# Optimization experiments

Measured on AMD Instinct MI355X. Metric: run time of the kernel, lower is better.

The kernel has to match this reference:

```python
import jax, jax.numpy as jnp
import numpy as np

N_NODES = 50000
N_EDGES = 800000
F_IN, F_LAT, F_OUT = 64, 64, 64


def _graph_conv(x, W, b, src, dst, deg_out_isqrt, deg_in_isqrt):
    # DGL GraphConv, norm='both': D_out^{-1/2} scaling on src side,
    # linear transform (mult-first since in_feats >= out_feats),
    # scatter-sum to dst, D_in^{-1/2} scaling on dst side, + bias.
    n = x.shape[0]
    h = (x * deg_out_isqrt[:, None]) @ W              # [N, F_out]
    msg = h[src]                                      # [E, F_out] gather
    agg = jax.ops.segment_sum(msg, dst, num_segments=n)  # [N, F_out] scatter
    return agg * deg_in_isqrt[:, None] + b


def setup_inputs() -> dict:
    key = jax.random.key(0)
    ks = jax.random.split(key, 6)
    x = jax.random.normal(ks[0], (N_NODES, F_IN), dtype=jnp.float32)
    W1 = jax.random.normal(ks[1], (F_IN, F_LAT), dtype=jnp.float32) / np.sqrt(F_IN)
    b1 = jnp.zeros((F_LAT,), dtype=jnp.float32)
    W2 = jax.random.normal(ks[2], (F_LAT, F_OUT), dtype=jnp.float32) / np.sqrt(F_LAT)
    b2 = jnp.zeros((F_OUT,), dtype=jnp.float32)
    src = jax.random.randint(ks[3], (N_EDGES,), 0, N_NODES, dtype=jnp.int32)
    dst = jax.random.randint(ks[4], (N_EDGES,), 0, N_NODES, dtype=jnp.int32)
    return {"x": x, "W1": W1, "b1": b1, "W2": W2, "b2": b2, "src": src, "dst": dst}


def reference(x, W1, b1, W2, b2, src, dst):
    n = x.shape[0]
    ones = jnp.ones((src.shape[0],), dtype=x.dtype)
    deg_out = jax.ops.segment_sum(ones, src, num_segments=n)
    deg_in = jax.ops.segment_sum(ones, dst, num_segments=n)
    deg_out_isqrt = jnp.where(deg_out > 0, jax.lax.rsqrt(jnp.maximum(deg_out, 1.0)), 0.0)
    deg_in_isqrt = jnp.where(deg_in > 0, jax.lax.rsqrt(jnp.maximum(deg_in, 1.0)), 0.0)
    h = _graph_conv(x, W1, b1, src, dst, deg_out_isqrt, deg_in_isqrt)
    h = jax.nn.relu(h)
    out = _graph_conv(h, W2, b2, src, dst, deg_out_isqrt, deg_in_isqrt)
    return out
```

## Files before the change

kernel.cpp:

```cpp
#include <hip/hip_runtime.h>

#define NF 64
#define BC 64
#define RANGE 16384
#define RWORDS (RANGE / 4)

typedef __attribute__((ext_vector_type(8))) short short8;
typedef __attribute__((ext_vector_type(4))) float floatx4;

__device__ __forceinline__ unsigned short f2bf(float f) {
  unsigned int u = __float_as_uint(f);
  return (unsigned short)((u + 0x7fffu + ((u >> 16) & 1u)) >> 16);
}

__global__ __launch_bounds__(256) void hist_kernel(
    const int* __restrict__ src, const int* __restrict__ dst,
    unsigned char* __restrict__ Gout, unsigned char* __restrict__ Gin,
    unsigned char* __restrict__ rank, int n, int nE, int R, int chunk) {
  __shared__ int cnt[RWORDS];
  const int rb = blockIdx.x % (R * BC);
  const int kind = blockIdx.x / (R * BC);
  const int r = rb / BC, b = rb % BC;
  const int r0 = r * RANGE;
  for (int i = threadIdx.x; i < RWORDS; i += 256) cnt[i] = 0;
  __syncthreads();
  const int lo = b * chunk, hi = min(lo + chunk, nE);
  const int* keys = kind ? src : dst;
  const int n4 = (hi > lo) ? ((hi - lo) >> 2) : 0;
  const int4* keys4 = (const int4*)(keys + lo);
  if (kind == 0) {
    for (int i = threadIdx.x; i < n4; i += 256) {
      int4 v = keys4[i];
      int e0 = lo + 4 * i;
      unsigned int k, old, sh;
      k = (unsigned int)(v.x - r0);
      if (k < (unsigned int)RANGE) { sh = (k & 3) * 8; old = atomicAdd(&cnt[k >> 2], 1u << sh); rank[e0 + 0] = (unsigned char)(old >> sh); }
      k = (unsigned int)(v.y - r0);
      if (k < (unsigned int)RANGE) { sh = (k & 3) * 8; old = atomicAdd(&cnt[k >> 2], 1u << sh); rank[e0 + 1] = (unsigned char)(old >> sh); }
      k = (unsigned int)(v.z - r0);
      if (k < (unsigned int)RANGE) { sh = (k & 3) * 8; old = atomicAdd(&cnt[k >> 2], 1u << sh); rank[e0 + 2] = (unsigned char)(old >> sh); }
      k = (unsigned int)(v.w - r0);
      if (k < (unsigned int)RANGE) { sh = (k & 3) * 8; old = atomicAdd(&cnt[k >> 2], 1u << sh); rank[e0 + 3] = (unsigned char)(old >> sh); }
    }
    for (int e = lo + 4 * n4 + threadIdx.x; e < hi; e += 256) {
      unsigned int k = (unsigned int)(keys[e] - r0);
      if (k < (unsigned int)RANGE) {
        unsigned int sh = (k & 3) * 8;
        unsigned int old = atomicAdd(&cnt[k >> 2], 1u << sh);
        rank[e] = (unsigned char)(old >> sh);
      }
    }
    __syncthreads();
    unsigned int* Gw = (unsigned int*)(Gin + (size_t)b * n + r0);
    for (int i = threadIdx.x; i < RWORDS; i += 256)
      if (r0 + 4 * i < n) Gw[i] = (unsigned int)cnt[i];
  } else {
    for (int i = threadIdx.x; i < n4; i += 256) {
      int4 v = keys4[i];
      unsigned int k;
      k = (unsigned int)(v.x - r0);
      if (k < (unsigned int)RANGE) atomicAdd(&cnt[k >> 2], 1u << ((k & 3) * 8));
      k = (unsigned int)(v.y - r0);
      if (k < (unsigned int)RANGE) atomicAdd(&cnt[k >> 2], 1u << ((k & 3) * 8));
      k = (unsigned int)(v.z - r0);
      if (k < (unsigned int)RANGE) atomicAdd(&cnt[k >> 2], 1u << ((k & 3) * 8));
      k = (unsigned int)(v.w - r0);
      if (k < (unsigned int)RANGE) atomicAdd(&cnt[k >> 2], 1u << ((k & 3) * 8));
    }
    for (int e = lo + 4 * n4 + threadIdx.x; e < hi; e += 256) {
      unsigned int k = (unsigned int)(keys[e] - r0);
      if (k < (unsigned int)RANGE) atomicAdd(&cnt[k >> 2], 1u << ((k & 3) * 8));
    }
    __syncthreads();
    unsigned int* Gw = (unsigned int*)(Gout + (size_t)b * n + r0);
    for (int i = threadIdx.x; i < RWORDS; i += 256)
      if (r0 + 4 * i < n) Gw[i] = (unsigned int)cnt[i];
  }
}

__global__ __launch_bounds__(256) void colscan_scan1_kernel(
    unsigned char* __restrict__ Gin, const unsigned char* __restrict__ Gout,
    float* __restrict__ so, float* __restrict__ si,
    int* __restrict__ lscan, int* __restrict__ bsum, int n) {
  __shared__ int s[256];
  const int tid = threadIdx.x;
  const int i = blockIdx.x * 256 + tid;
  int di = 0;
  if (i < n) {
    int base = 0;
    #pragma unroll 8
    for (int b = 0; b < BC; ++b) {
      int c = Gin[(size_t)b * n + i];
      Gin[(size_t)b * n + i] = (unsigned char)base;
      base += c;
    }
    di = base;
    int dsum = 0;
    #pragma unroll 8
    for (int b = 0; b < BC; ++b) dsum += Gout[(size_t)b * n + i];
    si[i] = di > 0 ? rsqrtf((float)di) : 0.f;
    so[i] = dsum > 0 ? rsqrtf((float)dsum) : 0.f;
  }
  s[tid] = di;
  __syncthreads();
  #pragma unroll
  for (int off = 1; off < 256; off <<= 1) {
    int t2 = (tid >= off) ? s[tid - off] : 0;
    __syncthreads();
    s[tid] += t2;
    __syncthreads();
  }
  if (i < n) lscan[i] = s[tid] - di;
  if (tid == 255) bsum[blockIdx.x] = s[255];
}

__global__ __launch_bounds__(256) void scan3_kernel(
    const int* __restrict__ lscan, const int* __restrict__ bsum,
    int* __restrict__ row_start, int n, int nE) {
  __shared__ int red[256];
  const int tid = threadIdx.x;
  const int b = blockIdx.x;
  red[tid] = (tid < b) ? bsum[tid] : 0;
  __syncthreads();
  #pragma unroll
  for (int s = 128; s > 0; s >>= 1) {
    if (tid < s) red[tid] += red[tid + s];
    __syncthreads();
  }
  const int off = red[0];
  const int i = b * 256 + tid;
  if (b == 0 && tid == 0) row_start[n] = nE;
  if (i < n) row_start[i] = lscan[i] + off;
}

__global__ __launch_bounds__(256) void basefill_kernel(
    const int* __restrict__ row_start, const unsigned char* __restrict__ Gin,
    int* __restrict__ base, int n, int nb) {
  const int c = blockIdx.x / nb;
  const int i = (blockIdx.x % nb) * 256 + threadIdx.x;
  if (i < n) base[(size_t)c * n + i] = row_start[i] + (int)Gin[(size_t)c * n + i];
}

__device__ __forceinline__ void mfma_gemm_core(
    const unsigned short* __restrict__ Ab, const unsigned short* __restrict__ Wt,
    unsigned short* __restrict__ H, int row0, int n, int t) {
  const int w = t >> 6, lane = t & 63;
  const int quad = lane >> 4, l15 = lane & 15;
  const short8 a0 = *(const short8*)&Ab[(w * 16 + l15) * 72 + quad * 8];
  const short8 a1 = *(const short8*)&Ab[(w * 16 + l15) * 72 + 32 + quad * 8];
  #pragma unroll
  for (int cg = 0; cg < 4; ++cg) {
    const short8 b0 = *(const short8*)&Wt[(cg * 16 + l15) * 72 + quad * 8];
    const short8 b1 = *(const short8*)&Wt[(cg * 16 + l15) * 72 + 32 + quad * 8];
    floatx4 acc = {0.f, 0.f, 0.f, 0.f};
    acc = __builtin_amdgcn_mfma_f32_16x16x32_bf16(a0, b0, acc, 0, 0, 0);
    acc = __builtin_amdgcn_mfma_f32_16x16x32_bf16(a1, b1, acc, 0, 0, 0);
    #pragma unroll
    for (int reg = 0; reg < 4; ++reg) {
      int grow = row0 + w * 16 + quad * 4 + reg;
      if (grow < n) H[(size_t)grow * NF + cg * 16 + l15] = f2bf(acc[reg]);
    }
  }
}

__device__ __forceinline__ void stage_wt(
    const float* __restrict__ W, unsigned short* __restrict__ Wt, int t) {
  #pragma unroll
  for (int i = 0; i < 16; ++i) {
    int idx = t + 256 * i;
    int k = idx >> 6, j = idx & 63;
    Wt[j * 72 + k] = f2bf(W[idx]);
  }
}

__global__ __launch_bounds__(256) void place_gemm1_kernel(
    const float* __restrict__ A, const float* __restrict__ so,
    const float* __restrict__ W, unsigned short* __restrict__ H, int n, int ggrid,
    const int* __restrict__ src, const int* __restrict__ dst,
    const unsigned char* __restrict__ rank, const int* __restrict__ base,
    unsigned short* __restrict__ sorted, int nE, int chunk) {
  __shared__ __align__(16) unsigned short Ab[64 * 72];
  __shared__ __align__(16) unsigned short Wt[64 * 72];
  const int t = threadIdx.x;
  if ((int)blockIdx.x >= ggrid) {
    int e = (blockIdx.x - ggrid) * 256 + t;
    if (e < nE) {
      int d = dst[e];
      int b = e / chunk;
      sorted[base[(size_t)b * n + d] + (int)rank[e]] = (unsigned short)src[e];
    }
    return;
  }
  stage_wt(W, Wt, t);
  const int row0 = blockIdx.x * 64;
  #pragma unroll
  for (int i = 0; i < 4; ++i) {
    int idx = t + 256 * i;
    int r = idx >> 4, c4 = idx & 15;
    int gr = row0 + r;
    float4 v = {0.f, 0.f, 0.f, 0.f};
    float s = 0.f;
    if (gr < n) {
      v = *(const float4*)&A[(size_t)gr * NF + c4 * 4];
      s = so[gr];
    }
    ushort4 o;
    o.x = f2bf(v.x * s); o.y = f2bf(v.y * s);
    o.z = f2bf(v.z * s); o.w = f2bf(v.w * s);
    *(ushort4*)&Ab[r * 72 + c4 * 4] = o;
  }
  __syncthreads();
  mfma_gemm_core(Ab, Wt, H, row0, n, t);
}

__global__ __launch_bounds__(256) void gemm2_kernel(
    const unsigned short* __restrict__ Tb, const float* __restrict__ W,
    unsigned short* __restrict__ H, int n) {
  __shared__ __align__(16) unsigned short Ab[64 * 72];
  __shared__ __align__(16) unsigned short Wt[64 * 72];
  const int t = threadIdx.x;
  stage_wt(W, Wt, t);
  const int row0 = blockIdx.x * 64;
  #pragma unroll
  for (int i = 0; i < 4; ++i) {
    int idx = t + 256 * i;
    int r = idx >> 4, c4 = idx & 15;
    int gr = row0 + r;
    ushort4 v = {0, 0, 0, 0};
    if (gr < n) v = *(const ushort4*)&Tb[(size_t)gr * NF + c4 * 4];
    *(ushort4*)&Ab[r * 72 + c4 * 4] = v;
  }
  __syncthreads();
  mfma_gemm_core(Ab, Wt, H, row0, n, t);
}

__device__ __forceinline__ void gather_sum(
    const unsigned short* __restrict__ H, const unsigned short* __restrict__ srcs,
    int beg, int end, int g, int c, float* acc) {
  const float4* Hv = (const float4*)H;
  int e = beg;
  for (; e + 16 <= end; e += 16) {
    int ia = srcs[e + g];
    int ib = srcs[e + 8 + g];
    float4 va = Hv[(size_t)ia * 8 + c];
    float4 vb = Hv[(size_t)ib * 8 + c];
    const unsigned int* pa = (const unsigned int*)&va;
    const unsigned int* pb = (const unsigned int*)&vb;
    #pragma unroll
    for (int k = 0; k < 4; ++k) {
      acc[2 * k]     += __uint_as_float(pa[k] << 16) + __uint_as_float(pb[k] << 16);
      acc[2 * k + 1] += __uint_as_float(pa[k] & 0xffff0000u) + __uint_as_float(pb[k] & 0xffff0000u);
    }
  }
  if (e + 8 <= end) {
    int ia = srcs[e + g];
    float4 va = Hv[(size_t)ia * 8 + c];
    const unsigned int* pa = (const unsigned int*)&va;
    #pragma unroll
    for (int k = 0; k < 4; ++k) {
      acc[2 * k]     += __uint_as_float(pa[k] << 16);
      acc[2 * k + 1] += __uint_as_float(pa[k] & 0xffff0000u);
    }
    e += 8;
  }
  if (e < end) {
    int idx = (e + g < end) ? (e + g) : (end - 1);
    float m = (e + g < end) ? 1.f : 0.f;
    int ia = srcs[idx];
    float4 va = Hv[(size_t)ia * 8 + c];
    const unsigned int* pa = (const unsigned int*)&va;
    #pragma unroll
    for (int k = 0; k < 4; ++k) {
      acc[2 * k]     += m * __uint_as_float(pa[k] << 16);
      acc[2 * k + 1] += m * __uint_as_float(pa[k] & 0xffff0000u);
    }
  }
  #pragma unroll
  for (int d = 8; d <= 32; d <<= 1) {
    #pragma unroll
    for (int k = 0; k < 8; ++k) acc[k] += __shfl_xor(acc[k], d);
  }
}

__global__ __launch_bounds__(256) void agg1_kernel(
    const unsigned short* __restrict__ H1, const int* __restrict__ row_start,
    const unsigned short* __restrict__ srcs, const float* __restrict__ si,
    const float* __restrict__ so, const float* __restrict__ b1,
    unsigned short* __restrict__ T, int n) {
  int node = blockIdx.x * 4 + (threadIdx.x >> 6);
  if (node >= n) return;
  const int lane = threadIdx.x & 63;
  const int g = lane >> 3;
  const int c = lane & 7;
  float acc[8] = {0, 0, 0, 0, 0, 0, 0, 0};
  gather_sum(H1, srcs, row_start[node], row_start[node + 1], g, c, acc);
  if (g == 0) {
    const float sin = si[node];
    const float son = so[node];
    ushort4 o0, o1;
    float v;
    v = fmaxf(fmaf(acc[0], sin, b1[c * 8 + 0]), 0.f) * son; o0.x = f2bf(v);
    v = fmaxf(fmaf(acc[1], sin, b1[c * 8 + 1]), 0.f) * son; o0.y = f2bf(v);
    v = fmaxf(fmaf(acc[2], sin, b1[c * 8 + 2]), 0.f) * son; o0.z = f2bf(v);
    v = fmaxf(fmaf(acc[3], sin, b1[c * 8 + 3]), 0.f) * son; o0.w = f2bf(v);
    v = fmaxf(fmaf(acc[4], sin, b1[c * 8 + 4]), 0.f) * son; o1.x = f2bf(v);
    v = fmaxf(fmaf(acc[5], sin, b1[c * 8 + 5]), 0.f) * son; o1.y = f2bf(v);
    v = fmaxf(fmaf(acc[6], sin, b1[c * 8 + 6]), 0.f) * son; o1.z = f2bf(v);
    v = fmaxf(fmaf(acc[7], sin, b1[c * 8 + 7]), 0.f) * son; o1.w = f2bf(v);
    *(ushort4*)&T[(size_t)node * NF + c * 8]     = o0;
    *(ushort4*)&T[(size_t)node * NF + c * 8 + 4] = o1;
  }
}

__global__ __launch_bounds__(256) void agg2_kernel(
    const unsigned short* __restrict__ H2, const int* __restrict__ row_start,
    const unsigned short* __restrict__ srcs, const float* __restrict__ si,
    const float* __restrict__ b2, float* __restrict__ out, int n) {
  int node = blockIdx.x * 4 + (threadIdx.x >> 6);
  if (node >= n) return;
  const int lane = threadIdx.x & 63;
  const int g = lane >> 3;
  const int c = lane & 7;
  float acc[8] = {0, 0, 0, 0, 0, 0, 0, 0};
  gather_sum(H2, srcs, row_start[node], row_start[node + 1], g, c, acc);
  if (g == 0) {
    const float sin = si[node];
    const float4 b4a = *(const float4*)&b2[c * 8];
    const float4 b4b = *(const float4*)&b2[c * 8 + 4];
    float4 r0, r1;
    r0.x = fmaf(acc[0], sin, b4a.x);
    r0.y = fmaf(acc[1], sin, b4a.y);
    r0.z = fmaf(acc[2], sin, b4a.z);
    r0.w = fmaf(acc[3], sin, b4a.w);
    r1.x = fmaf(acc[4], sin, b4b.x);
    r1.y = fmaf(acc[5], sin, b4b.y);
    r1.z = fmaf(acc[6], sin, b4b.z);
    r1.w = fmaf(acc[7], sin, b4b.w);
    *(float4*)&out[(size_t)node * NF + c * 8]     = r0;
    *(float4*)&out[(size_t)node * NF + c * 8 + 4] = r1;
  }
}

extern "C" void kernel_launch(void* const* d_in, const int* in_sizes, int n_in,
                              void* d_out, int out_size, void* d_ws, size_t ws_size,
                              hipStream_t stream) {
  const float* x  = (const float*)d_in[0];
  const float* W1 = (const float*)d_in[1];
  const float* b1 = (const float*)d_in[2];
  const float* W2 = (const float*)d_in[3];
  const float* b2 = (const float*)d_in[4];
  const int* src  = (const int*)d_in[5];
  const int* dst  = (const int*)d_in[6];
  float* out = (float*)d_out;

  const int N = in_sizes[0] / NF;
  const int E = in_sizes[5];
  const int NB = (N + 255) / 256;
  const int R  = (N + RANGE - 1) / RANGE;
  const int CH = (((E + BC - 1) / BC) + 3) & ~3;
  (void)ws_size;

  char* ws = (char*)d_ws;
  size_t p = 0;
  auto alloc = [&](size_t bytes) -> void* {
    void* r = ws + p;
    p = (p + bytes + 255) & ~(size_t)255;
    return r;
  };
  float* so         = (float*)alloc((size_t)N * 4);
  float* si         = (float*)alloc((size_t)N * 4);
  int*   row_start  = (int*)  alloc((size_t)(N + 1) * 4);
  int*   bsum       = (int*)  alloc((size_t)NB * 4);
  int*   lscan      = (int*)  alloc((size_t)N * 4);
  unsigned short* sorted_u16 = (unsigned short*)alloc((size_t)E * 2);
  unsigned char*  rank  = (unsigned char*)alloc((size_t)E);
  unsigned short* h1    = (unsigned short*)alloc((size_t)N * NF * 2);
  unsigned char*  G_in  = (unsigned char*)alloc((size_t)BC * N);
  unsigned char*  G_out = (unsigned char*)alloc((size_t)BC * N);
  unsigned short* tb    = (unsigned short*)alloc((size_t)N * NF * 2);
  int*            base  = (int*)alloc((size_t)BC * N * 4);
  unsigned short* h2 = h1;

  hist_kernel<<<2 * R * BC, 256, 0, stream>>>(src, dst, G_out, G_in, rank,
                                              N, E, R, CH);

  colscan_scan1_kernel<<<NB, 256, 0, stream>>>(G_in, G_out, so, si,
                                               lscan, bsum, N);

  scan3_kernel<<<NB, 256, 0, stream>>>(lscan, bsum, row_start, N, E);

  basefill_kernel<<<BC * NB, 256, 0, stream>>>(row_start, G_in, base, N, NB);

  const int ggrid = (N + 63) / 64;
  const int pgrid = (E + 255) / 256;
  const int agrid = (N + 3) / 4;

  place_gemm1_kernel<<<ggrid + pgrid, 256, 0, stream>>>(
      x, so, W1, h1, N, ggrid, src, dst, rank, base, sorted_u16, E, CH);

  agg1_kernel<<<agrid, 256, 0, stream>>>(h1, row_start, sorted_u16, si, so, b1, tb, N);

  gemm2_kernel<<<ggrid, 256, 0, stream>>>(tb, W2, h2, N);

  agg2_kernel<<<agrid, 256, 0, stream>>>(h2, row_start, sorted_u16, si, b2, out, N);
}
```

Measured before the change: 183.8 us.

## Fuse second GEMM into aggregation, merge scan with basefill, halve histogram chunks

Layer 2 now aggregates the scaled activations first and applies W2 per node afterwards, using an FP32 shared-memory matvec inside agg2. This removes the separate gemm2 kernel and the h2 round trip. The scan3 and basefill kernels are merged into one launch. The histogram uses 32 chunks with 512-thread blocks, down from 64 chunks with 256 threads. The cost is a 64x64 matvec per node computed on scalar FP32 in the aggregation kernel, a 16 KB W2 load per block, and a block-wide sync.

```diff
diff --git a/kernel.cpp b/kernel.cpp
--- a/kernel.cpp
+++ b/kernel.cpp
@@ -1,7 +1,7 @@
 #include <hip/hip_runtime.h>
 
 #define NF 64
-#define BC 64
+#define BC 32
 #define RANGE 16384
 #define RWORDS (RANGE / 4)
 
@@ -13,7 +13,7 @@
   return (unsigned short)((u + 0x7fffu + ((u >> 16) & 1u)) >> 16);
 }
 
-__global__ __launch_bounds__(256) void hist_kernel(
+__global__ __launch_bounds__(512) void hist_kernel(
     const int* __restrict__ src, const int* __restrict__ dst,
     unsigned char* __restrict__ Gout, unsigned char* __restrict__ Gin,
     unsigned char* __restrict__ rank, int n, int nE, int R, int chunk) {
@@ -22,14 +22,14 @@
   const int kind = blockIdx.x / (R * BC);
   const int r = rb / BC, b = rb % BC;
   const int r0 = r * RANGE;
-  for (int i = threadIdx.x; i < RWORDS; i += 256) cnt[i] = 0;
+  for (int i = threadIdx.x; i < RWORDS; i += 512) cnt[i] = 0;
   __syncthreads();
   const int lo = b * chunk, hi = min(lo + chunk, nE);
   const int* keys = kind ? src : dst;
   const int n4 = (hi > lo) ? ((hi - lo) >> 2) : 0;
   const int4* keys4 = (const int4*)(keys + lo);
   if (kind == 0) {
-    for (int i = threadIdx.x; i < n4; i += 256) {
+    for (int i = threadIdx.x; i < n4; i += 512) {
       int4 v = keys4[i];
       int e0 = lo + 4 * i;
       unsigned int k, old, sh;
@@ -42,7 +42,7 @@
       k = (unsigned int)(v.w - r0);
       if (k < (unsigned int)RANGE) { sh = (k & 3) * 8; old = atomicAdd(&cnt[k >> 2], 1u << sh); rank[e0 + 3] = (unsigned char)(old >> sh); }
     }
-    for (int e = lo + 4 * n4 + threadIdx.x; e < hi; e += 256) {
+    for (int e = lo + 4 * n4 + threadIdx.x; e < hi; e += 512) {
       unsigned int k = (unsigned int)(keys[e] - r0);
       if (k < (unsigned int)RANGE) {
         unsigned int sh = (k & 3) * 8;
@@ -52,10 +52,10 @@
     }
     __syncthreads();
     unsigned int* Gw = (unsigned int*)(Gin + (size_t)b * n + r0);
-    for (int i = threadIdx.x; i < RWORDS; i += 256)
+    for (int i = threadIdx.x; i < RWORDS; i += 512)
       if (r0 + 4 * i < n) Gw[i] = (unsigned int)cnt[i];
   } else {
-    for (int i = threadIdx.x; i < n4; i += 256) {
+    for (int i = threadIdx.x; i < n4; i += 512) {
       int4 v = keys4[i];
       unsigned int k;
       k = (unsigned int)(v.x - r0);
@@ -67,13 +67,13 @@
       k = (unsigned int)(v.w - r0);
       if (k < (unsigned int)RANGE) atomicAdd(&cnt[k >> 2], 1u << ((k & 3) * 8));
     }
-    for (int e = lo + 4 * n4 + threadIdx.x; e < hi; e += 256) {
+    for (int e = lo + 4 * n4 + threadIdx.x; e < hi; e += 512) {
       unsigned int k = (unsigned int)(keys[e] - r0);
       if (k < (unsigned int)RANGE) atomicAdd(&cnt[k >> 2], 1u << ((k & 3) * 8));
     }
     __syncthreads();
     unsigned int* Gw = (unsigned int*)(Gout + (size_t)b * n + r0);
-    for (int i = threadIdx.x; i < RWORDS; i += 256)
+    for (int i = threadIdx.x; i < RWORDS; i += 512)
       if (r0 + 4 * i < n) Gw[i] = (unsigned int)cnt[i];
   }
 }
@@ -114,13 +114,15 @@
   if (tid == 255) bsum[blockIdx.x] = s[255];
 }
 
-__global__ __launch_bounds__(256) void scan3_kernel(
+__global__ __launch_bounds__(256) void scan3_basefill_kernel(
     const int* __restrict__ lscan, const int* __restrict__ bsum,
-    int* __restrict__ row_start, int n, int nE) {
+    const unsigned char* __restrict__ Gin, int* __restrict__ row_start,
+    int* __restrict__ base, int n, int nb, int nE) {
   __shared__ int red[256];
   const int tid = threadIdx.x;
-  const int b = blockIdx.x;
-  red[tid] = (tid < b) ? bsum[tid] : 0;
+  const int c = blockIdx.x / nb;
+  const int ib = blockIdx.x % nb;
+  red[tid] = (tid < ib) ? bsum[tid] : 0;
   __syncthreads();
   #pragma unroll
   for (int s = 128; s > 0; s >>= 1) {
@@ -128,17 +130,13 @@
     __syncthreads();
   }
   const int off = red[0];
-  const int i = b * 256 + tid;
-  if (b == 0 && tid == 0) row_start[n] = nE;
-  if (i < n) row_start[i] = lscan[i] + off;
-}
-
-__global__ __launch_bounds__(256) void basefill_kernel(
-    const int* __restrict__ row_start, const unsigned char* __restrict__ Gin,
-    int* __restrict__ base, int n, int nb) {
-  const int c = blockIdx.x / nb;
-  const int i = (blockIdx.x % nb) * 256 + threadIdx.x;
-  if (i < n) base[(size_t)c * n + i] = row_start[i] + (int)Gin[(size_t)c * n + i];
+  const int i = ib * 256 + tid;
+  if (i < n) {
+    const int rs = lscan[i] + off;
+    if (c == 0) row_start[i] = rs;
+    base[(size_t)c * n + i] = rs + (int)Gin[(size_t)c * n + i];
+  }
+  if (c == 0 && ib == 0 && tid == 0) row_start[n] = nE;
 }
 
 __device__ __forceinline__ void mfma_gemm_core(
@@ -208,27 +206,6 @@
     o.x = f2bf(v.x * s); o.y = f2bf(v.y * s);
     o.z = f2bf(v.z * s); o.w = f2bf(v.w * s);
     *(ushort4*)&Ab[r * 72 + c4 * 4] = o;
-  }
-  __syncthreads();
-  mfma_gemm_core(Ab, Wt, H, row0, n, t);
-}
-
-__global__ __launch_bounds__(256) void gemm2_kernel(
-    const unsigned short* __restrict__ Tb, const float* __restrict__ W,
-    unsigned short* __restrict__ H, int n) {
-  __shared__ __align__(16) unsigned short Ab[64 * 72];
-  __shared__ __align__(16) unsigned short Wt[64 * 72];
-  const int t = threadIdx.x;
-  stage_wt(W, Wt, t);
-  const int row0 = blockIdx.x * 64;
-  #pragma unroll
-  for (int i = 0; i < 4; ++i) {
-    int idx = t + 256 * i;
-    int r = idx >> 4, c4 = idx & 15;
-    int gr = row0 + r;
-    ushort4 v = {0, 0, 0, 0};
-    if (gr < n) v = *(const ushort4*)&Tb[(size_t)gr * NF + c4 * 4];
-    *(ushort4*)&Ab[r * 72 + c4 * 4] = v;
   }
   __syncthreads();
   mfma_gemm_core(Ab, Wt, H, row0, n, t);
@@ -313,31 +290,35 @@
 }
 
 __global__ __launch_bounds__(256) void agg2_kernel(
-    const unsigned short* __restrict__ H2, const int* __restrict__ row_start,
+    const unsigned short* __restrict__ Tb, const int* __restrict__ row_start,
     const unsigned short* __restrict__ srcs, const float* __restrict__ si,
-    const float* __restrict__ b2, float* __restrict__ out, int n) {
-  int node = blockIdx.x * 4 + (threadIdx.x >> 6);
-  if (node >= n) return;
-  const int lane = threadIdx.x & 63;
+    const float* __restrict__ W2, const float* __restrict__ b2,
+    float* __restrict__ out, int n) {
+  __shared__ __align__(16) float W2s[64 * 64];
+  __shared__ float u[4][64];
+  const int t = threadIdx.x;
+  #pragma unroll
+  for (int i = 0; i < 4; ++i)
+    *(float4*)&W2s[t * 4 + 1024 * i] = *(const float4*)&W2[t * 4 + 1024 * i];
+  const int w = t >> 6;
+  const int lane = t & 63;
   const int g = lane >> 3;
   const int c = lane & 7;
+  const int node = blockIdx.x * 4 + w;
+  const bool valid = node < n;
   float acc[8] = {0, 0, 0, 0, 0, 0, 0, 0};
-  gather_sum(H2, srcs, row_start[node], row_start[node + 1], g, c, acc);
+  if (valid) gather_sum(Tb, srcs, row_start[node], row_start[node + 1], g, c, acc);
   if (g == 0) {
-    const float sin = si[node];
-    const float4 b4a = *(const float4*)&b2[c * 8];
-    const float4 b4b = *(const float4*)&b2[c * 8 + 4];
-    float4 r0, r1;
-    r0.x = fmaf(acc[0], sin, b4a.x);
-    r0.y = fmaf(acc[1], sin, b4a.y);
-    r0.z = fmaf(acc[2], sin, b4a.z);
-    r0.w = fmaf(acc[3], sin, b4a.w);
-    r1.x = fmaf(acc[4], sin, b4b.x);
-    r1.y = fmaf(acc[5], sin, b4b.y);
-    r1.z = fmaf(acc[6], sin, b4b.z);
-    r1.w = fmaf(acc[7], sin, b4b.w);
-    *(float4*)&out[(size_t)node * NF + c * 8]     = r0;
-    *(float4*)&out[(size_t)node * NF + c * 8 + 4] = r1;
+    const float sin = valid ? si[node] : 0.f;
+    #pragma unroll
+    for (int k = 0; k < 8; ++k) u[w][c * 8 + k] = acc[k] * sin;
+  }
+  __syncthreads();
+  if (valid) {
+    float r = b2[lane];
+    #pragma unroll
+    for (int k = 0; k < 64; ++k) r = fmaf(u[w][k], W2s[k * 64 + lane], r);
+    out[(size_t)node * NF + lane] = r;
   }
 }
 
@@ -379,17 +360,15 @@
   unsigned char*  G_out = (unsigned char*)alloc((size_t)BC * N);
   unsigned short* tb    = (unsigned short*)alloc((size_t)N * NF * 2);
   int*            base  = (int*)alloc((size_t)BC * N * 4);
-  unsigned short* h2 = h1;
-
-  hist_kernel<<<2 * R * BC, 256, 0, stream>>>(src, dst, G_out, G_in, rank,
+
+  hist_kernel<<<2 * R * BC, 512, 0, stream>>>(src, dst, G_out, G_in, rank,
                                               N, E, R, CH);
 
   colscan_scan1_kernel<<<NB, 256, 0, stream>>>(G_in, G_out, so, si,
                                                lscan, bsum, N);
 
-  scan3_kernel<<<NB, 256, 0, stream>>>(lscan, bsum, row_start, N, E);
-
-  basefill_kernel<<<BC * NB, 256, 0, stream>>>(row_start, G_in, base, N, NB);
+  scan3_basefill_kernel<<<BC * NB, 256, 0, stream>>>(lscan, bsum, G_in,
+                                                     row_start, base, N, NB, E);
 
   const int ggrid = (N + 63) / 64;
   const int pgrid = (E + 255) / 256;
@@ -400,7 +379,5 @@
 
   agg1_kernel<<<agrid, 256, 0, stream>>>(h1, row_start, sorted_u16, si, so, b1, tb, N);
 
-  gemm2_kernel<<<ggrid, 256, 0, stream>>>(tb, W2, h2, N);
-
-  agg2_kernel<<<agrid, 256, 0, stream>>>(h2, row_start, sorted_u16, si, b2, out, N);
-}
+  agg2_kernel<<<agrid, 256, 0, stream>>>(tb, row_start, sorted_u16, si, W2, b2, out, N);
+}
```

Result: no change. 180.9 us (-1.6%).
